# Optimization experiments

Measured on AMD Instinct MI355X. Metric: run time of the kernel, lower is better.

## Reference

```python
import jax, jax.numpy as jnp
import numpy as np
import math

EPS = 1e-11

def _gaussian_kernel3():
    # fixed 3x3 gaussian, mean=(3-1)/2=1, variance=0.5^2
    coords = jnp.arange(3, dtype=jnp.float32)
    xg = jnp.tile(coords[None, :], (3, 1))  # x_cord.repeat(3).view(3,3)
    yg = xg.T
    variance = 0.25
    g = (1.0 / (2.0 * math.pi * variance)) * jnp.exp(-((xg - 1.0) ** 2 + (yg - 1.0) ** 2) / (2.0 * variance))
    return g  # (3,3)

def setup_inputs() -> dict:
    key = jax.random.key(0)
    k1, k2 = jax.random.split(key)
    b, cin, h, w = 8, 512, 16, 16
    cout = 128
    x = jax.random.normal(k1, (b, cin, h, w), dtype=jnp.float32)
    w_conv = jax.random.normal(k2, (cout, cin), dtype=jnp.float32) * (1.0 / np.sqrt(cin))
    return {"x": x, "w_conv": w_conv}

def reference(x, w_conv):
    # 1x1 conv (no bias) + relu
    y = jnp.einsum('bihw,oi->bohw', x, w_conv)
    y = jax.nn.relu(y)
    # depthwise 3x3 gaussian blur, VALID padding (matches nn.Conv2d default padding=0)
    c = w_conv.shape[0]
    gk = _gaussian_kernel3()
    dw = jnp.tile(gk[None, None], (c, 1, 1, 1))  # (C,1,3,3)
    y = jax.lax.conv_general_dilated(
        y, dw, window_strides=(1, 1), padding='VALID',
        dimension_numbers=('NCHW', 'OIHW', 'NCHW'), feature_group_count=c)
    b, c, h, w = y.shape
    hw = h * w
    xf = y.reshape(b, c, hw)
    # shifted copies: xs[b, ch, i, p] = xf[b, ch, (p - i) mod hw]
    p = jnp.arange(hw)
    idx = (p[None, :] - p[:, None]) % hw  # (hw_i, hw_p)
    xs = xf[:, :, idx]  # [b, c, hw, hw]
    # responses[b, ch1, ch2, p] = sum_i xf[b,ch1,i] * xf[b,ch2,(p-i)%hw]
    R = jnp.einsum('bai,bcip->bacp', xf, xs)  # [b, c, c, hw]
    # faithful torch reshape: [b, c, c*hw] -> view(b, hw, c*c), max over dim 1
    resp = R.reshape(b, hw, c * c)
    c_ij = jnp.sqrt(jnp.max(resp, axis=1))  # [b, c*c]
    norm = jnp.sum(c_ij ** 2, axis=1, keepdims=True) + EPS
    return c_ij / norm
```

## Files before the change

### kernel.cpp

```cpp
#include <hip/hip_runtime.h>
#include <hip/hip_bf16.h>

typedef __bf16 bf16x8 __attribute__((ext_vector_type(8)));
typedef float floatx4 __attribute__((ext_vector_type(4)));
typedef unsigned short u16;
typedef unsigned int u32;

#define HW 196
#define KP2 232
#define CL 432
#define NB 8
#define NC 128
#define WROW 12544

__global__ __launch_bounds__(512) void k_stage1(const float* __restrict__ x,
                                                const float* __restrict__ wc,
                                                __hip_bfloat16* __restrict__ xf,
                                                __hip_bfloat16* __restrict__ xfr) {
  const int b   = blockIdx.x;
  const int og  = blockIdx.y;
  const int t   = threadIdx.x;
  const int pix = t & 255;
  const int half = t >> 8;
  const float* xb = x + ((size_t)(b * 512 + half * 256)) * 256 + pix;
  const float* w0 = wc + og * 4 * 512 + half * 256;

  float a0 = 0.f, a1 = 0.f, a2 = 0.f, a3 = 0.f;
#pragma unroll 16
  for (int i = 0; i < 256; ++i) {
    float xv = xb[(size_t)i * 256];
    a0 = fmaf(xv, w0[i], a0);
    a1 = fmaf(xv, w0[512 + i], a1);
    a2 = fmaf(xv, w0[1024 + i], a2);
    a3 = fmaf(xv, w0[1536 + i], a3);
  }

  __shared__ float ybuf[4][512];
  ybuf[0][t] = a0; ybuf[1][t] = a1; ybuf[2][t] = a2; ybuf[3][t] = a3;
  __syncthreads();

  if (t < 256) {
#pragma unroll
    for (int oo = 0; oo < 4; ++oo)
      ybuf[oo][t] = fmaxf(ybuf[oo][t] + ybuf[oo][256 + t], 0.f);
  }
  __syncthreads();

  const float GC = 0.63661977236758138f;
  const float GE = GC * 0.13533528323661270f;
  const float GD = GC * 0.018315638888734179f;

  if (t < KP2) {
    int h = 0, w2 = 0;
    if (t < HW) { h = t / 14; w2 = t - h * 14; }
#pragma unroll
    for (int oo = 0; oo < 4; ++oo) {
      float v = 0.f;
      if (t < HW) {
        const float* yb = &ybuf[oo][h * 16 + w2];
        v = GD * (yb[0] + yb[2] + yb[32] + yb[34])
          + GE * (yb[1] + yb[16] + yb[18] + yb[33])
          + GC * yb[17];
      }
      const int row = b * NC + og * 4 + oo;
      __hip_bfloat16 bv = __float2bfloat16(v);
      xf[row * KP2 + t] = bv;
      const int ir = (t < HW) ? ((t == 0) ? 0 : (HW - t)) : t;
      xfr[row * KP2 + ir] = bv;
    }
  }
}

__global__ __launch_bounds__(256, 2) void k_cooc(const __hip_bfloat16* __restrict__ xf,
                                                 const __hip_bfloat16* __restrict__ xfr,
                                                 u32* __restrict__ W) {
  const int b     = blockIdx.x;
  const int cpair = blockIdx.y;
  const int t     = threadIdx.x;

  __shared__ __align__(16) u16 Abuf[NC * KP2];
  __shared__ __align__(16) u16 ext[8 * CL];
  __shared__ __align__(16) u16 Obuf[32 * 200];

  {
    const uint4* src = (const uint4*)(xfr + (size_t)b * NC * KP2);
    uint4* dst = (uint4*)Abuf;
    for (int j = t; j < NC * KP2 / 8; j += 256) dst[j] = src[j];
  }
  __syncthreads();

  const int lane = t & 63;
  const int wv   = t >> 6;
  const int n    = lane & 15;
  const int quad = lane >> 4;
  const int S    = n & 7;
  const int extoff = S * CL + (n & 8) + quad * 8;
  const int arow   = n * KP2 + quad * 8;

  for (int c2 = 0; c2 < 2; ++c2) {
    const int c = cpair * 2 + c2;

    {
      const u16* xfu = (const u16*)xf + (b * NC + c) * KP2;
      for (int j = t; j < 8 * CL; j += 256) {
        const int Sh = j / CL;
        const int m = j - Sh * CL;
        int idx = m + Sh;
        if (idx >= 2 * HW) idx -= 2 * HW; else if (idx >= HW) idx -= HW;
        ext[j] = xfu[idx];
      }
    }
    __syncthreads();

    floatx4 acc[8][4];
#pragma unroll
    for (int at = 0; at < 8; ++at)
#pragma unroll
      for (int j = 0; j < 4; ++j) acc[at][j] = (floatx4){0.f, 0.f, 0.f, 0.f};

    for (int kb = 0; kb < 7; ++kb) {
      const int i0 = kb * 32;
      bf16x8 af[8];
#pragma unroll
      for (int at = 0; at < 8; ++at)
        af[at] = *((const bf16x8*)&Abuf[(at * 16) * KP2 + arow + i0]);

#define DO_PT(JC)                                                                \
      {                                                                          \
        const int p0 = (wv + 4 * (JC)) * 16;                                     \
        const bf16x8 bv = *((const bf16x8*)&ext[extoff + p0 + i0]);              \
        _Pragma("unroll")                                                        \
        for (int at = 0; at < 8; ++at)                                           \
          acc[at][JC] = __builtin_amdgcn_mfma_f32_16x16x32_bf16(af[at], bv,      \
                                                                acc[at][JC], 0, 0, 0); \
      }
      DO_PT(0)
      DO_PT(1)
      DO_PT(2)
      if (wv == 0) { DO_PT(3) }
#undef DO_PT
    }

#define EPI(JC)                                                                  \
    {                                                                            \
      const int p = (wv + 4 * (JC)) * 16 + n;                                    \
      if (p < HW) {                                                              \
        _Pragma("unroll")                                                        \
        for (int a0t = 0; a0t < 2; ++a0t) {                                      \
          _Pragma("unroll")                                                      \
          for (int rr = 0; rr < 4; ++rr) {                                       \
            float v = fmaxf(fmaxf(acc[a0t][JC][rr], acc[a0t + 2][JC][rr]),       \
                            fmaxf(acc[a0t + 4][JC][rr], acc[a0t + 6][JC][rr]));  \
            const int a1 = a0t * 16 + quad * 4 + rr;                             \
            union { __hip_bfloat16 h; u16 u; } cv;                               \
            cv.h = __float2bfloat16(v);                                          \
            Obuf[a1 * 200 + p] = cv.u;                                           \
          }                                                                      \
        }                                                                        \
      }                                                                          \
    }
    EPI(0)
    EPI(1)
    EPI(2)
    if (wv == 0) { EPI(3) }
#undef EPI
    __syncthreads();

    {
      const u32* O32 = (const u32*)Obuf;
      u32* Wb = W + ((size_t)b * 32) * WROW + c * 98;
      for (int j = t; j < 32 * 98; j += 256) {
        const int row = (int)(((unsigned)j * 10700u) >> 20);
        const int col = j - row * 98;
        Wb[row * WROW + col] = O32[row * 100 + col];
      }
    }
    __syncthreads();
  }
}

__global__ __launch_bounds__(256) void k_max(const u32* __restrict__ W,
                                             float* __restrict__ out,
                                             float* __restrict__ sums) {
  const int gid = blockIdx.x * 256 + threadIdx.x;
  const int b  = gid >> 13;
  const int r0 = (gid & 8191) << 1;
  const u32* Wb = W + (size_t)b * 32 * WROW;

  float m0 = 0.f, m1 = 0.f;
#pragma unroll 4
  for (int a1 = 0; a1 < 32; ++a1) {
    const int s = (r0 - ((a1 * 8704) & 16383)) & 16383;
    const u32 v = Wb[a1 * WROW + (s >> 1)];
    m0 = fmaxf(m0, __uint_as_float((v & 0xffffu) << 16));
    m1 = fmaxf(m1, __uint_as_float(v & 0xffff0000u));
    if (s < 8704) {
      const u32 v2 = Wb[a1 * WROW + ((s + 16384) >> 1)];
      m0 = fmaxf(m0, __uint_as_float((v2 & 0xffffu) << 16));
      m1 = fmaxf(m1, __uint_as_float(v2 & 0xffff0000u));
    }
  }
  const int o = b * 16384 + r0;
  out[o]     = sqrtf(m0);
  out[o + 1] = sqrtf(m1);

  float s2 = m0 + m1;
#pragma unroll
  for (int off = 32; off > 0; off >>= 1) s2 += __shfl_down(s2, off, 64);
  __shared__ float part[4];
  if ((threadIdx.x & 63) == 0) part[threadIdx.x >> 6] = s2;
  __syncthreads();
  if (threadIdx.x == 0)
    atomicAdd(&sums[b], part[0] + part[1] + part[2] + part[3]);
}

__global__ __launch_bounds__(256) void k_norm(const float* __restrict__ sums,
                                              float* __restrict__ out) {
  const int gid = blockIdx.x * 256 + threadIdx.x;
  const int b = gid >> 14;
  out[gid] = out[gid] / (sums[b] + 1e-11f);
}

extern "C" void kernel_launch(void* const* d_in, const int* in_sizes, int n_in,
                              void* d_out, int out_size, void* d_ws, size_t ws_size,
                              hipStream_t stream) {
  const float* x  = (const float*)d_in[0];
  const float* wc = (const float*)d_in[1];

  char* ws = (char*)d_ws;
  __hip_bfloat16* xf  = (__hip_bfloat16*)ws;
  __hip_bfloat16* xfr = (__hip_bfloat16*)(ws + 475136);
  u32* W      = (u32*)(ws + 950272);
  float* sums = (float*)(ws + 950272 + 12845056);

  hipMemsetAsync(sums, 0, NB * sizeof(float), stream);
  k_stage1<<<dim3(NB, 32), 512, 0, stream>>>(x, wc, xf, xfr);
  k_cooc<<<dim3(NB, 64), 256, 0, stream>>>(xf, xfr, W);
  k_max<<<256, 256, 0, stream>>>(W, (float*)d_out, sums);
  k_norm<<<(NB * 16384) / 256, 256, 0, stream>>>(sums, (float*)d_out);
}
```

Before: 118.7 us.

## Pre-swizzle MFMA operands in stage1 and read shifted B tiles from global

Stage1 now computes 8 output channels per block and writes two layouts. One is the reversed A operand, pre-swizzled into the MFMA fragment order. The other is an 8-shift expanded copy of each channel. k_cooc then loads A fragments with a contiguous per-lane uint4 read and reads B fragments directly from global memory. This removes the per-channel LDS construction of the shifted buffer and its barrier. In exchange the B operands come from global or cache rather than LDS, and the workspace grows for the expanded copy.

Result: slower. 138.0 us (+16.2%).

```diff
diff --git a/kernel.cpp b/kernel.cpp
--- a/kernel.cpp
+++ b/kernel.cpp
@@ -7,41 +7,43 @@
 typedef unsigned int u32;
 
 #define HW 196
-#define KP2 232
-#define CL 432
 #define NB 8
 #define NC 128
+#define CL 480
 #define WROW 12544
+
+#define OFF_XFRSW 0
+#define OFF_XFE   458752
+#define OFF_W     8323072
+#define OFF_SUMS  21168128
 
 __global__ __launch_bounds__(512) void k_stage1(const float* __restrict__ x,
                                                 const float* __restrict__ wc,
-                                                __hip_bfloat16* __restrict__ xf,
-                                                __hip_bfloat16* __restrict__ xfr) {
+                                                uint4* __restrict__ xfr_sw,
+                                                u16* __restrict__ xfe) {
   const int b   = blockIdx.x;
   const int og  = blockIdx.y;
   const int t   = threadIdx.x;
   const int pix = t & 255;
   const int half = t >> 8;
   const float* xb = x + ((size_t)(b * 512 + half * 256)) * 256 + pix;
-  const float* w0 = wc + og * 4 * 512 + half * 256;
-
-  float a0 = 0.f, a1 = 0.f, a2 = 0.f, a3 = 0.f;
-#pragma unroll 16
+  const float* w0 = wc + og * 8 * 512 + half * 256;
+
+  float a[8] = {0.f, 0.f, 0.f, 0.f, 0.f, 0.f, 0.f, 0.f};
+#pragma unroll 8
   for (int i = 0; i < 256; ++i) {
     float xv = xb[(size_t)i * 256];
-    a0 = fmaf(xv, w0[i], a0);
-    a1 = fmaf(xv, w0[512 + i], a1);
-    a2 = fmaf(xv, w0[1024 + i], a2);
-    a3 = fmaf(xv, w0[1536 + i], a3);
-  }
-
-  __shared__ float ybuf[4][512];
-  ybuf[0][t] = a0; ybuf[1][t] = a1; ybuf[2][t] = a2; ybuf[3][t] = a3;
-  __syncthreads();
-
+#pragma unroll
+    for (int oo = 0; oo < 8; ++oo) a[oo] = fmaf(xv, w0[oo * 512 + i], a[oo]);
+  }
+
+  __shared__ float ybuf[8][512];
+#pragma unroll
+  for (int oo = 0; oo < 8; ++oo) ybuf[oo][t] = a[oo];
+  __syncthreads();
   if (t < 256) {
 #pragma unroll
-    for (int oo = 0; oo < 4; ++oo)
+    for (int oo = 0; oo < 8; ++oo)
       ybuf[oo][t] = fmaxf(ybuf[oo][t] + ybuf[oo][256 + t], 0.f);
   }
   __syncthreads();
@@ -50,42 +52,63 @@
   const float GE = GC * 0.13533528323661270f;
   const float GD = GC * 0.018315638888734179f;
 
-  if (t < KP2) {
-    int h = 0, w2 = 0;
-    if (t < HW) { h = t / 14; w2 = t - h * 14; }
-#pragma unroll
-    for (int oo = 0; oo < 4; ++oo) {
-      float v = 0.f;
-      if (t < HW) {
-        const float* yb = &ybuf[oo][h * 16 + w2];
-        v = GD * (yb[0] + yb[2] + yb[32] + yb[34])
-          + GE * (yb[1] + yb[16] + yb[18] + yb[33])
-          + GC * yb[17];
-      }
-      const int row = b * NC + og * 4 + oo;
-      __hip_bfloat16 bv = __float2bfloat16(v);
-      xf[row * KP2 + t] = bv;
-      const int ir = (t < HW) ? ((t == 0) ? 0 : (HW - t)) : t;
-      xfr[row * KP2 + ir] = bv;
-    }
-  }
-}
-
-__global__ __launch_bounds__(256, 2) void k_cooc(const __hip_bfloat16* __restrict__ xf,
-                                                 const __hip_bfloat16* __restrict__ xfr,
+  __shared__ u16 ydup[8][592];
+  if (t < HW) {
+    const int h = t / 14, w2 = t - h * 14;
+#pragma unroll
+    for (int oo = 0; oo < 8; ++oo) {
+      const float* yb = &ybuf[oo][h * 16 + w2];
+      float v = GD * (yb[0] + yb[2] + yb[32] + yb[34])
+              + GE * (yb[1] + yb[16] + yb[18] + yb[33])
+              + GC * yb[17];
+      union { __hip_bfloat16 h2; u16 u; } cv; cv.h2 = __float2bfloat16(v);
+      ydup[oo][t] = cv.u; ydup[oo][t + 196] = cv.u; ydup[oo][t + 392] = cv.u;
+    }
+  }
+  __syncthreads();
+
+  if (t < 224) {
+    const int oo = t / 28;
+    const int g  = t - oo * 28;
+    const int kb = g >> 2, quad = g & 3;
+    const int c  = og * 8 + oo;
+    const int at = c >> 4, m = c & 15;
+    union { u16 u[8]; uint4 v; } pk;
+#pragma unroll
+    for (int j = 0; j < 8; ++j) {
+      const int k = g * 8 + j;
+      pk.u[j] = (k < HW) ? ydup[oo][HW - k] : (u16)0;
+    }
+    xfr_sw[b * 3584 + ((kb * 8 + at) * 4 + quad) * 16 + m] = pk.v;
+  }
+
+  uint4* xfe4 = (uint4*)xfe;
+  for (int idx = t; idx < 8 * 8 * 60; idx += 512) {
+    const int oo = idx / 480;
+    const int rem = idx - oo * 480;
+    const int S = rem / 60;
+    const int g = rem - S * 60;
+    const int c = og * 8 + oo;
+    union { u16 u[8]; uint4 v; } pk;
+#pragma unroll
+    for (int j = 0; j < 8; ++j) pk.u[j] = ydup[oo][g * 8 + j + S];
+    xfe4[((size_t)(b * NC + c) * 8 + S) * 60 + g] = pk.v;
+  }
+}
+
+__global__ __launch_bounds__(256, 2) void k_cooc(const uint4* __restrict__ xfr_sw,
+                                                 const u16* __restrict__ xfe,
                                                  u32* __restrict__ W) {
   const int b     = blockIdx.x;
   const int cpair = blockIdx.y;
   const int t     = threadIdx.x;
 
-  __shared__ __align__(16) u16 Abuf[NC * KP2];
-  __shared__ __align__(16) u16 ext[8 * CL];
+  __shared__ __align__(16) uint4 Abuf[3584];
   __shared__ __align__(16) u16 Obuf[32 * 200];
 
   {
-    const uint4* src = (const uint4*)(xfr + (size_t)b * NC * KP2);
-    uint4* dst = (uint4*)Abuf;
-    for (int j = t; j < NC * KP2 / 8; j += 256) dst[j] = src[j];
+    const uint4* src = xfr_sw + b * 3584;
+    for (int j = t; j < 3584; j += 256) Abuf[j] = src[j];
   }
   __syncthreads();
 
@@ -93,24 +116,12 @@
   const int wv   = t >> 6;
   const int n    = lane & 15;
   const int quad = lane >> 4;
-  const int S    = n & 7;
-  const int extoff = S * CL + (n & 8) + quad * 8;
-  const int arow   = n * KP2 + quad * 8;
+  const u16* xbase = xfe + ((size_t)(b * NC) * 8) * CL + (n & 8) + quad * 8
+                   + (size_t)(n & 7) * CL;
 
   for (int c2 = 0; c2 < 2; ++c2) {
     const int c = cpair * 2 + c2;
-
-    {
-      const u16* xfu = (const u16*)xf + (b * NC + c) * KP2;
-      for (int j = t; j < 8 * CL; j += 256) {
-        const int Sh = j / CL;
-        const int m = j - Sh * CL;
-        int idx = m + Sh;
-        if (idx >= 2 * HW) idx -= 2 * HW; else if (idx >= HW) idx -= HW;
-        ext[j] = xfu[idx];
-      }
-    }
-    __syncthreads();
+    const u16* xc = xbase + (size_t)c * (8 * CL);
 
     floatx4 acc[8][4];
 #pragma unroll
@@ -119,16 +130,15 @@
       for (int j = 0; j < 4; ++j) acc[at][j] = (floatx4){0.f, 0.f, 0.f, 0.f};
 
     for (int kb = 0; kb < 7; ++kb) {
-      const int i0 = kb * 32;
       bf16x8 af[8];
 #pragma unroll
       for (int at = 0; at < 8; ++at)
-        af[at] = *((const bf16x8*)&Abuf[(at * 16) * KP2 + arow + i0]);
+        af[at] = *((const bf16x8*)&Abuf[(kb * 8 + at) * 64 + lane]);
 
 #define DO_PT(JC)                                                                \
       {                                                                          \
         const int p0 = (wv + 4 * (JC)) * 16;                                     \
-        const bf16x8 bv = *((const bf16x8*)&ext[extoff + p0 + i0]);              \
+        const bf16x8 bv = *((const bf16x8*)&xc[p0 + kb * 32]);                   \
         _Pragma("unroll")                                                        \
         for (int at = 0; at < 8; ++at)                                           \
           acc[at][JC] = __builtin_amdgcn_mfma_f32_16x16x32_bf16(af[at], bv,      \
@@ -228,14 +238,14 @@
   const float* wc = (const float*)d_in[1];
 
   char* ws = (char*)d_ws;
-  __hip_bfloat16* xf  = (__hip_bfloat16*)ws;
-  __hip_bfloat16* xfr = (__hip_bfloat16*)(ws + 475136);
-  u32* W      = (u32*)(ws + 950272);
-  float* sums = (float*)(ws + 950272 + 12845056);
+  uint4* xfr_sw = (uint4*)(ws + OFF_XFRSW);
+  u16*   xfe    = (u16*)(ws + OFF_XFE);
+  u32*   W      = (u32*)(ws + OFF_W);
+  float* sums   = (float*)(ws + OFF_SUMS);
 
   hipMemsetAsync(sums, 0, NB * sizeof(float), stream);
-  k_stage1<<<dim3(NB, 32), 512, 0, stream>>>(x, wc, xf, xfr);
-  k_cooc<<<dim3(NB, 64), 256, 0, stream>>>(xf, xfr, W);
+  k_stage1<<<dim3(NB, 16), 512, 0, stream>>>(x, wc, xfr_sw, xfe);
+  k_cooc<<<dim3(NB, 64), 256, 0, stream>>>(xfr_sw, xfe, W);
   k_max<<<256, 256, 0, stream>>>(W, (float*)d_out, sums);
   k_norm<<<(NB * 16384) / 256, 256, 0, stream>>>(sums, (float*)d_out);
 }
```
